# Performance work log

Hardware: AMD Instinct MI355X
Metric: run time of the kernel (lower is better)

Reference implementation:

```python
import jax, jax.numpy as jnp
import numpy as np

B, T, D, H = 2, 2048, 1024, 16
HD = D // H


def setup_inputs() -> dict:
    key = jax.random.key(0)
    ks = jax.random.split(key, 9)
    s = 1.0 / np.sqrt(D)
    return {
        "x": jax.random.normal(ks[0], (B, T, D), dtype=jnp.float32),
        "Wq": jax.random.normal(ks[1], (D, D), dtype=jnp.float32) * s,
        "bq": jnp.zeros((D,), dtype=jnp.float32),
        "Wk": jax.random.normal(ks[2], (D, D), dtype=jnp.float32) * s,
        "bk": jnp.zeros((D,), dtype=jnp.float32),
        "Wv": jax.random.normal(ks[3], (D, D), dtype=jnp.float32) * s,
        "bv": jnp.zeros((D,), dtype=jnp.float32),
        "Wo": jax.random.normal(ks[4], (D, D), dtype=jnp.float32) * s,
        "bo": jnp.zeros((D,), dtype=jnp.float32),
    }


def reference(x, Wq, bq, Wk, bk, Wv, bv, Wo, bo):
    b, t, d = x.shape
    # projections, split heads: (b, h, t, hd)
    def heads(y):
        return y.reshape(b, t, H, HD).transpose(0, 2, 1, 3)
    Q = heads(x @ Wq + bq)
    K = heads(x @ Wk + bk)
    V = heads(x @ Wv + bv)
    # scores scaled by sqrt(d) (full embed dim, faithful to source)
    score = jnp.einsum("bhid,bhjd->bhij", Q, K) / jnp.sqrt(jnp.float32(d))
    causal = jnp.triu(jnp.ones((t, t), dtype=bool), k=1)  # (t, t)
    score = jnp.where(causal, jnp.float32(-1e10), score)
    # FAITHFUL quirk: softmax over the HEAD axis (torch dim=1 of [b,h,t,t])
    weight = jax.nn.softmax(score, axis=1)
    out = jnp.einsum("bhij,bhjd->bhid", weight, V)
    out = out.transpose(0, 2, 1, 3).reshape(b, t, d)
    return out @ Wo + bo
```

## Files before the change

### kernel.cpp

```cpp
#include <hip/hip_runtime.h>
#include <hip/hip_bf16.h>

#define B_ 2
#define T_ 2048
#define D_ 1024
#define H_ 16

typedef __attribute__((ext_vector_type(8))) short bf16x8;
typedef __attribute__((ext_vector_type(4))) short bf16x4;
typedef __attribute__((ext_vector_type(4))) float f32x4;

__device__ __forceinline__ unsigned pack_bf16(float x, float y) {
  unsigned xb = __float_as_uint(x), yb = __float_as_uint(y);
  xb += 0x7fffu + ((xb >> 16) & 1u);
  yb += 0x7fffu + ((yb >> 16) & 1u);
  return (xb >> 16) | (yb & 0xffff0000u);
}
__device__ __forceinline__ unsigned short f2b(float x) {
  unsigned u = __float_as_uint(x);
  u += 0x7fffu + ((u >> 16) & 1u);
  return (unsigned short)(u >> 16);
}
__device__ __forceinline__ float blo(unsigned u) { return __uint_as_float(u << 16); }
__device__ __forceinline__ float bhi(unsigned u) { return __uint_as_float(u & 0xffff0000u); }

__device__ __forceinline__ void gld_lds16(const unsigned short* g, unsigned short* l) {
  __builtin_amdgcn_global_load_lds(
      (const __attribute__((address_space(1))) unsigned int*)g,
      (__attribute__((address_space(3))) unsigned int*)l, 16, 0, 0);
}

__global__ __launch_bounds__(256) void wtrans(const float* __restrict__ W0, const float* __restrict__ W1,
                                              const float* __restrict__ W2, const float* __restrict__ W3,
                                              unsigned short* __restrict__ T0, unsigned short* __restrict__ T1,
                                              unsigned short* __restrict__ T2, unsigned short* __restrict__ T3) {
  const int z = blockIdx.z;
  const float* W = z == 0 ? W0 : z == 1 ? W1 : z == 2 ? W2 : W3;
  unsigned short* T = z == 0 ? T0 : z == 1 ? T1 : z == 2 ? T2 : T3;
  __shared__ unsigned short t[64][72];
  const int k0 = blockIdx.x << 6, n0 = blockIdx.y << 6;
  const int r = threadIdx.x >> 2, c16 = (threadIdx.x & 3) << 4;
#pragma unroll
  for (int e = 0; e < 4; ++e) {
    const float4 v = *(const float4*)&W[(size_t)(k0 + r) * 1024 + n0 + c16 + e * 4];
    t[r][c16 + e * 4 + 0] = f2b(v.x);
    t[r][c16 + e * 4 + 1] = f2b(v.y);
    t[r][c16 + e * 4 + 2] = f2b(v.z);
    t[r][c16 + e * 4 + 3] = f2b(v.w);
  }
  __syncthreads();
  unsigned short o[16];
#pragma unroll
  for (int e = 0; e < 16; ++e) o[e] = t[c16 + e][r];
  unsigned short* dst = &T[(size_t)(n0 + r) * 1024 + k0 + c16];
  *(uint4*)&dst[0] = *(uint4*)&o[0];
  *(uint4*)&dst[8] = *(uint4*)&o[8];
}

__global__ __launch_bounds__(256) void xconv(const float* __restrict__ x, unsigned short* __restrict__ xb) {
  const int i = (blockIdx.x * 256 + threadIdx.x) * 8;
  const float4 a = *(const float4*)&x[i];
  const float4 b = *(const float4*)&x[i + 4];
  uint4 o;
  o.x = pack_bf16(a.x, a.y);
  o.y = pack_bf16(a.z, a.w);
  o.z = pack_bf16(b.x, b.y);
  o.w = pack_bf16(b.z, b.w);
  *(uint4*)&xb[i] = o;
}

template <bool BF16OUT>
__global__ __launch_bounds__(256) void gemm_mfma(const unsigned short* __restrict__ A,
                                                 const unsigned short* __restrict__ B0,
                                                 const unsigned short* __restrict__ B1,
                                                 const unsigned short* __restrict__ B2,
                                                 const float* __restrict__ bi0, const float* __restrict__ bi1,
                                                 const float* __restrict__ bi2,
                                                 void* __restrict__ Y0, void* __restrict__ Y1,
                                                 void* __restrict__ Y2) {
  const int z = blockIdx.z;
  const unsigned short* Bt = z == 0 ? B0 : z == 1 ? B1 : B2;
  const float* bias = z == 0 ? bi0 : z == 1 ? bi1 : bi2;
  void* Y = z == 0 ? Y0 : z == 1 ? Y1 : Y2;
  __shared__ unsigned short As[8192];
  __shared__ unsigned short Bs[8192];
  const int tid = threadIdx.x;
  const int m0 = blockIdx.y << 7, n0 = blockIdx.x << 7;
  const int w = tid >> 6, l = tid & 63, g = l >> 4, c = l & 15;
  const int wm = (w >> 1) << 6, wn = (w & 1) << 6;
  const int srow = tid >> 3;
  const int skel = ((tid & 7) ^ (srow & 7)) << 3;
  const unsigned short* ga = &A[(size_t)(m0 + srow) * 1024 + skel];
  const unsigned short* gb = &Bt[(size_t)(n0 + srow) * 1024 + skel];
  unsigned short* la = &As[tid << 3];
  unsigned short* lb = &Bs[tid << 3];
  f32x4 acc[4][4];
#pragma unroll
  for (int i = 0; i < 4; ++i)
#pragma unroll
    for (int j = 0; j < 4; ++j) acc[i][j] = {0.f, 0.f, 0.f, 0.f};
  for (int k0 = 0; k0 < 1024; k0 += 64) {
    __syncthreads();
#pragma unroll
    for (int a = 0; a < 4; ++a) {
      gld_lds16(ga + (size_t)(a << 5) * 1024 + k0, la + (a << 11));
      gld_lds16(gb + (size_t)(a << 5) * 1024 + k0, lb + (a << 11));
    }
    __syncthreads();
#pragma unroll
    for (int kc = 0; kc < 2; ++kc) {
      bf16x8 af[4], bfr[4];
#pragma unroll
      for (int mf = 0; mf < 4; ++mf) {
        const int m = wm + (mf << 4) + c;
        af[mf] = *(const bf16x8*)&As[((m << 6) + (kc << 5) + (g << 3)) ^ ((m & 7) << 3)];
      }
#pragma unroll
      for (int nf = 0; nf < 4; ++nf) {
        const int n = wn + (nf << 4) + c;
        bfr[nf] = *(const bf16x8*)&Bs[((n << 6) + (kc << 5) + (g << 3)) ^ ((n & 7) << 3)];
      }
#pragma unroll
      for (int mf = 0; mf < 4; ++mf)
#pragma unroll
        for (int nf = 0; nf < 4; ++nf)
          acc[mf][nf] = __builtin_amdgcn_mfma_f32_16x16x32_bf16(af[mf], bfr[nf], acc[mf][nf], 0, 0, 0);
    }
  }
#pragma unroll
  for (int nf = 0; nf < 4; ++nf) {
    const int n = n0 + wn + (nf << 4) + c;
    const float bb = bias[n];
#pragma unroll
    for (int mf = 0; mf < 4; ++mf) {
      const int mrow = m0 + wm + (mf << 4) + (g << 2);
#pragma unroll
      for (int r = 0; r < 4; ++r) {
        const float val = acc[mf][nf][r] + bb;
        if (BF16OUT)
          ((unsigned short*)Y)[((size_t)(mrow + r) << 10) + n] = f2b(val);
        else
          ((float*)Y)[((size_t)(mrow + r) << 10) + n] = val;
      }
    }
  }
}

__global__ __launch_bounds__(256) void gemm_vt(const unsigned short* __restrict__ A,
                                               const unsigned short* __restrict__ Bt,
                                               const float* __restrict__ bias,
                                               unsigned short* __restrict__ Vt) {
  __shared__ unsigned short As[8192];
  __shared__ unsigned short Bs[8192];
  __shared__ unsigned short sm[128][136];
  const int tid = threadIdx.x;
  const int m0 = blockIdx.y << 7, n0 = blockIdx.x << 7;
  const int w = tid >> 6, l = tid & 63, g = l >> 4, c = l & 15;
  const int wm = (w >> 1) << 6, wn = (w & 1) << 6;
  const int srow = tid >> 3;
  const int skel = ((tid & 7) ^ (srow & 7)) << 3;
  const unsigned short* ga = &A[(size_t)(m0 + srow) * 1024 + skel];
  const unsigned short* gb = &Bt[(size_t)(n0 + srow) * 1024 + skel];
  unsigned short* la = &As[tid << 3];
  unsigned short* lb = &Bs[tid << 3];
  f32x4 acc[4][4];
#pragma unroll
  for (int i = 0; i < 4; ++i)
#pragma unroll
    for (int j = 0; j < 4; ++j) acc[i][j] = {0.f, 0.f, 0.f, 0.f};
  for (int k0 = 0; k0 < 1024; k0 += 64) {
    __syncthreads();
#pragma unroll
    for (int a = 0; a < 4; ++a) {
      gld_lds16(ga + (size_t)(a << 5) * 1024 + k0, la + (a << 11));
      gld_lds16(gb + (size_t)(a << 5) * 1024 + k0, lb + (a << 11));
    }
    __syncthreads();
#pragma unroll
    for (int kc = 0; kc < 2; ++kc) {
      bf16x8 af[4], bfr[4];
#pragma unroll
      for (int mf = 0; mf < 4; ++mf) {
        const int m = wm + (mf << 4) + c;
        af[mf] = *(const bf16x8*)&As[((m << 6) + (kc << 5) + (g << 3)) ^ ((m & 7) << 3)];
      }
#pragma unroll
      for (int nf = 0; nf < 4; ++nf) {
        const int n = wn + (nf << 4) + c;
        bfr[nf] = *(const bf16x8*)&Bs[((n << 6) + (kc << 5) + (g << 3)) ^ ((n & 7) << 3)];
      }
#pragma unroll
      for (int mf = 0; mf < 4; ++mf)
#pragma unroll
        for (int nf = 0; nf < 4; ++nf)
          acc[mf][nf] = __builtin_amdgcn_mfma_f32_16x16x32_bf16(af[mf], bfr[nf], acc[mf][nf], 0, 0, 0);
    }
  }
  __syncthreads();
#pragma unroll
  for (int nf = 0; nf < 4; ++nf) {
    const int nl = wn + (nf << 4) + c;
    const float bb = bias[n0 + nl];
#pragma unroll
    for (int mf = 0; mf < 4; ++mf) {
      const int ml = wm + (mf << 4) + (g << 2);
      uint2 o;
      o.x = pack_bf16(acc[mf][nf][0] + bb, acc[mf][nf][1] + bb);
      o.y = pack_bf16(acc[mf][nf][2] + bb, acc[mf][nf][3] + bb);
      *(uint2*)&sm[nl][ml] = o;
    }
  }
  __syncthreads();
  const int bb2 = m0 >> 11, mr0 = m0 & 2047;
#pragma unroll
  for (int it = 0; it < 8; ++it) {
    const int u = tid + (it << 8);
    const int ns = u >> 4, mc = (u & 15) << 3;
    *(uint4*)&Vt[(((size_t)((bb2 << 10) + n0 + ns)) << 11) + mr0 + mc] = *(const uint4*)&sm[ns][mc];
  }
}

__global__ __launch_bounds__(256) void vblk32t(const unsigned short* __restrict__ Vt,
                                               float* __restrict__ Blk) {
  const int b = blockIdx.x >> 6, t = blockIdx.x & 63;
#pragma unroll
  for (int dd = 0; dd < 4; ++dd) {
    const int d = threadIdx.x + (dd << 8);
    const unsigned short* vr = &Vt[(((size_t)((b << 10) + d)) << 11) + (t << 5)];
    float s = 0.f;
#pragma unroll
    for (int qq = 0; qq < 4; ++qq) {
      const uint2 v0 = *(const uint2*)&vr[qq << 3];
      const uint2 v1 = *(const uint2*)&vr[(qq << 3) + 4];
      s += blo(v0.x) + bhi(v0.x) + blo(v0.y) + bhi(v0.y);
      s += blo(v1.x) + bhi(v1.x) + blo(v1.y) + bhi(v1.y);
    }
    Blk[(((size_t)((b << 6) + t)) << 10) + d] = s;
  }
}

__global__ __launch_bounds__(256) void vsuffix32(const float* __restrict__ Blk, float* __restrict__ Suf) {
  const int idx = blockIdx.x * 256 + threadIdx.x;
  const int b = idx >> 10, d = idx & 1023;
  float s = 0.f;
  Suf[((size_t)(b * 65 + 64) << 10) + d] = 0.f;
  for (int t = 63; t >= 0; --t) {
    s += Blk[((size_t)((b << 6) + t) << 10) + d];
    Suf[((size_t)(b * 65 + t) << 10) + d] = s;
  }
}

__global__ __launch_bounds__(1024, 4) void attn_v17(const unsigned short* __restrict__ Qb,
                                                    const unsigned short* __restrict__ Kb,
                                                    const unsigned short* __restrict__ Vt,
                                                    unsigned short* __restrict__ P0,
                                                    unsigned short* __restrict__ P1,
                                                    unsigned short* __restrict__ P2,
                                                    unsigned short* __restrict__ P3) {
  __shared__ unsigned short Ks[2][16 * 1024];
  __shared__ unsigned short Vs[2][1024 * 16];
  __shared__ uint2 Sx[2][8][64];

  const int combo = blockIdx.x;
  const int b = combo & 1, s = combo >> 1;
  const int qy = 63 - blockIdx.y;
  const int tid = threadIdx.x;
  const int w = tid >> 6, l = tid & 63, g = l >> 4, c = l & 15;
  const int isub = w >> 3, hp = w & 7;
  const float SC = 0.04508422f;
  unsigned short* AOp = s == 0 ? P0 : s == 1 ? P1 : s == 2 ? P2 : P3;

  const int krow0 = tid >> 7, kc8 = tid & 127;
  const int kscc0 = kc8 ^ (krow0 & 7);
  const int krow1 = krow0 + 8;
  const int kscc1 = kc8 ^ (krow1 & 7);
  const unsigned short* kp0 = &Kb[(((size_t)((b << 11) + krow0)) << 10) + (kscc0 << 3)];
  const unsigned short* kp1 = &Kb[(((size_t)((b << 11) + krow1)) << 10) + (kscc1 << 3)];
  const int vd0 = tid >> 1, vjc = tid & 1;
  const int vjo0 = ((vjc << 1) ^ (((vd0 >> 2) & 1) << 1)) << 2;
  const int vd1 = vd0 + 512;
  const int vjo1 = ((vjc << 1) ^ (((vd1 >> 2) & 1) << 1)) << 2;
  const unsigned short* vp0 = &Vt[(((size_t)((b << 10) + vd0)) << 11) + vjo0];
  const unsigned short* vp1 = &Vt[(((size_t)((b << 10) + vd1)) << 11) + vjo1];

#pragma unroll
  for (int ph = 0; ph < 2; ++ph) {
    const int q = ph ? (63 - qy) : qy;
    const int nt16 = (q + 1) << 1;
    const int i0w = (q << 5) + (isub << 4);
    const int ib = i0w + c;

    const unsigned short* qbase =
        &Qb[((size_t)((b << 11) + i0w + c) << 10) + (hp << 7) + (g << 3)];
    bf16x8 qf[4];
    qf[0] = *(const bf16x8*)&qbase[0];
    qf[1] = *(const bf16x8*)&qbase[32];
    qf[2] = *(const bf16x8*)&qbase[64];
    qf[3] = *(const bf16x8*)&qbase[96];

    f32x4 acc[2][4];
#pragma unroll
    for (int hh = 0; hh < 2; ++hh)
#pragma unroll
      for (int cc = 0; cc < 4; ++cc) acc[hh][cc] = {0.f, 0.f, 0.f, 0.f};

#pragma unroll
    for (int e = 0; e < 2; ++e) {
      const int eh = e ? (7 - s) : s;
      const int lo = eh << 4;
      const int hi = (lo + 16) < nt16 ? (lo + 16) : nt16;
      if (lo >= hi) continue;

      {
        const size_t ko = ((size_t)lo << 14);
        gld_lds16(kp0 + ko, &Ks[0][tid << 3]);
        gld_lds16(kp1 + ko, &Ks[0][(tid + 1024) << 3]);
        const int jo = lo << 4;
        gld_lds16(vp0 + jo, &Vs[0][tid << 3]);
        gld_lds16(vp1 + jo, &Vs[0][(tid + 1024) << 3]);
      }
      __syncthreads();

      for (int ts = lo; ts < hi; ++ts) {
        const int cur = (ts - lo) & 1;
        if (ts + 1 < hi) {
          const size_t ko = ((size_t)(ts + 1) << 14);
          gld_lds16(kp0 + ko, &Ks[cur ^ 1][tid << 3]);
          gld_lds16(kp1 + ko, &Ks[cur ^ 1][(tid + 1024) << 3]);
          const int jo = (ts + 1) << 4;
          gld_lds16(vp0 + jo, &Vs[cur ^ 1][tid << 3]);
          gld_lds16(vp1 + jo, &Vs[cur ^ 1][(tid + 1024) << 3]);
        }
        const int j0 = ts << 4;
        const int kx = c & 7;
        f32x4 ex[2];
        f32x4 ps = {0.f, 0.f, 0.f, 0.f};
#pragma unroll
        for (int hh = 0; hh < 2; ++hh) {
          const int hc = ((hp << 1) + hh) << 3;
          const bf16x8 k0 = *(const bf16x8*)&Ks[cur][((c << 7) + ((hc + g) ^ kx)) << 3];
          const bf16x8 k1 = *(const bf16x8*)&Ks[cur][((c << 7) + ((hc + 4 + g) ^ kx)) << 3];
          f32x4 a = {0.f, 0.f, 0.f, 0.f};
          a = __builtin_amdgcn_mfma_f32_16x16x32_bf16(k0, qf[2 * hh], a, 0, 0, 0);
          a = __builtin_amdgcn_mfma_f32_16x16x32_bf16(k1, qf[2 * hh + 1], a, 0, 0, 0);
#pragma unroll
          for (int r = 0; r < 4; ++r) ex[hh][r] = exp2f(a[r] * SC);
          ps += ex[hh];
        }
        uint2 pp;
        pp.x = pack_bf16(ps[0], ps[1]);
        pp.y = pack_bf16(ps[2], ps[3]);
        Sx[isub][hp][l] = pp;
        __syncthreads();
        f32x4 sum = {0.f, 0.f, 0.f, 0.f};
#pragma unroll
        for (int d8 = 0; d8 < 8; ++d8) {
          const uint2 u = Sx[isub][d8][l];
          sum[0] += blo(u.x);
          sum[1] += bhi(u.x);
          sum[2] += blo(u.y);
          sum[3] += bhi(u.y);
        }
        f32x4 inv;
#pragma unroll
        for (int r = 0; r < 4; ++r) inv[r] = __builtin_amdgcn_rcpf(sum[r]);
        float wv[2][4];
        if (j0 + 15 <= i0w) {
#pragma unroll
          for (int hh = 0; hh < 2; ++hh)
#pragma unroll
            for (int r = 0; r < 4; ++r) wv[hh][r] = ex[hh][r] * inv[r];
        } else {
          const int jb = j0 + (g << 2);
#pragma unroll
          for (int hh = 0; hh < 2; ++hh)
#pragma unroll
            for (int r = 0; r < 4; ++r)
              wv[hh][r] = (jb + r > ib) ? 0.0625f : ex[hh][r] * inv[r];
        }
#pragma unroll
        for (int hh = 0; hh < 2; ++hh) {
          union { bf16x4 v; unsigned u[2]; } pa;
          pa.u[0] = pack_bf16(wv[hh][0], wv[hh][1]);
          pa.u[1] = pack_bf16(wv[hh][2], wv[hh][3]);
#pragma unroll
          for (int cc = 0; cc < 4; ++cc) {
            const int d = (((hp << 1) + hh) << 6) + (cc << 4) + c;
            const int up = g ^ (((d >> 2) & 1) << 1);
            union { bf16x4 v; unsigned u[2]; } vf;
            *(uint2*)&vf = *(const uint2*)&Vs[cur][(d << 4) + (up << 2)];
            acc[hh][cc] =
                __builtin_amdgcn_mfma_f32_16x16x16bf16_1k(pa.v, vf.v, acc[hh][cc], 0, 0, 0);
          }
        }
        __syncthreads();
      }
    }
#pragma unroll
    for (int hh = 0; hh < 2; ++hh)
#pragma unroll
      for (int cc = 0; cc < 4; ++cc) {
        const int d = (((hp << 1) + hh) << 6) + (cc << 4) + c;
#pragma unroll
        for (int r = 0; r < 4; ++r)
          AOp[((size_t)((b << 11) + i0w + (g << 2) + r) << 10) + d] = f2b(acc[hh][cc][r]);
      }
  }
}

__global__ __launch_bounds__(256) void aocvt(const unsigned short* __restrict__ P0,
                                             const unsigned short* __restrict__ P1,
                                             const unsigned short* __restrict__ P2,
                                             const unsigned short* __restrict__ P3,
                                             const float* __restrict__ Suf,
                                             unsigned short* __restrict__ AOb) {
  const int i = (blockIdx.x * 256 + threadIdx.x) << 3;
  const int m = i >> 10;
  const int b = m >> 11;
  const int sufidx = ((m & 2047) >> 5) + 1;
  const int d0 = i & 1023;
  const float* sp = &Suf[((size_t)(b * 65 + sufidx) << 10) + d0];
  const uint4 v0 = *(const uint4*)&P0[i];
  const uint4 v1 = *(const uint4*)&P1[i];
  const uint4 v2 = *(const uint4*)&P2[i];
  const uint4 v3 = *(const uint4*)&P3[i];
  const float4 s0 = *(const float4*)&sp[0];
  const float4 s1 = *(const float4*)&sp[4];
  uint4 o;
  o.x = pack_bf16(blo(v0.x) + blo(v1.x) + blo(v2.x) + blo(v3.x) + 0.0625f * s0.x,
                  bhi(v0.x) + bhi(v1.x) + bhi(v2.x) + bhi(v3.x) + 0.0625f * s0.y);
  o.y = pack_bf16(blo(v0.y) + blo(v1.y) + blo(v2.y) + blo(v3.y) + 0.0625f * s0.z,
                  bhi(v0.y) + bhi(v1.y) + bhi(v2.y) + bhi(v3.y) + 0.0625f * s0.w);
  o.z = pack_bf16(blo(v0.z) + blo(v1.z) + blo(v2.z) + blo(v3.z) + 0.0625f * s1.x,
                  bhi(v0.z) + bhi(v1.z) + bhi(v2.z) + bhi(v3.z) + 0.0625f * s1.y);
  o.w = pack_bf16(blo(v0.w) + blo(v1.w) + blo(v2.w) + blo(v3.w) + 0.0625f * s1.z,
                  bhi(v0.w) + bhi(v1.w) + bhi(v2.w) + bhi(v3.w) + 0.0625f * s1.w);
  *(uint4*)&AOb[i] = o;
}

extern "C" void kernel_launch(void* const* d_in, const int* in_sizes, int n_in,
                              void* d_out, int out_size, void* d_ws, size_t ws_size,
                              hipStream_t stream) {
  (void)in_sizes; (void)n_in; (void)out_size; (void)ws_size;
  const float* x = (const float*)d_in[0];
  const float* Wq = (const float*)d_in[1];
  const float* bq = (const float*)d_in[2];
  const float* Wk = (const float*)d_in[3];
  const float* bk = (const float*)d_in[4];
  const float* Wv = (const float*)d_in[5];
  const float* bv = (const float*)d_in[6];
  const float* Wo = (const float*)d_in[7];
  const float* bo = (const float*)d_in[8];
  float* out = (float*)d_out;
  char* ws = (char*)d_ws;

  const size_t MB = 1024 * 1024;
  unsigned short* xb  = (unsigned short*)(ws);
  unsigned short* Qb  = (unsigned short*)(ws + 8 * MB);
  unsigned short* Kb  = (unsigned short*)(ws + 16 * MB);
  unsigned short* AOP1 = (unsigned short*)(ws + 24 * MB);
  unsigned short* Vt  = (unsigned short*)(ws + 32 * MB);
  unsigned short* Wqt = (unsigned short*)(ws + 40 * MB);
  unsigned short* Wkt = (unsigned short*)(ws + 42 * MB);
  unsigned short* Wvt = (unsigned short*)(ws + 44 * MB);
  unsigned short* Wot = (unsigned short*)(ws + 46 * MB);
  unsigned short* AOP2 = (unsigned short*)(ws + 48 * MB);
  unsigned short* AOP3 = (unsigned short*)(ws + 56 * MB);
  float* Blk = (float*)(ws + 40 * MB);
  float* Suf = (float*)(ws + 40 * MB + 512 * 1024);
  unsigned short* AOP0 = xb;
  unsigned short* AOb = Qb;

  hipLaunchKernelGGL(wtrans, dim3(16, 16, 4), dim3(256), 0, stream,
                     Wq, Wk, Wv, Wo, Wqt, Wkt, Wvt, Wot);
  hipLaunchKernelGGL(xconv, dim3(2048), dim3(256), 0, stream, x, xb);
  hipLaunchKernelGGL((gemm_mfma<true>), dim3(8, 32, 2), dim3(256), 0, stream,
                     xb, Wqt, Wkt, Wkt, bq, bk, bk, (void*)Qb, (void*)Kb, (void*)Kb);
  hipLaunchKernelGGL(gemm_vt, dim3(8, 32), dim3(256), 0, stream, xb, Wvt, bv, Vt);
  hipLaunchKernelGGL(vblk32t, dim3(128), dim3(256), 0, stream, Vt, Blk);
  hipLaunchKernelGGL(vsuffix32, dim3(8), dim3(256), 0, stream, Blk, Suf);
  hipLaunchKernelGGL(attn_v17, dim3(8, 32), dim3(1024), 0, stream,
                     Qb, Kb, Vt, AOP0, AOP1, AOP2, AOP3);
  hipLaunchKernelGGL(aocvt, dim3(2048), dim3(256), 0, stream,
                     AOP0, AOP1, AOP2, AOP3, Suf, AOb);
  hipLaunchKernelGGL((gemm_mfma<false>), dim3(8, 32, 1), dim3(256), 0, stream,
                     AOb, Wot, Wot, Wot, bo, bo, bo, (void*)out, (void*)out, (void*)out);
}
```

Measured before the change: 196.0 us.

## Fuse partial-sum reduction into output GEMM and use fp32 head-sum exchange

Removes the separate aocvt pass by folding the reduction of the four attention partial outputs plus the suffix term into the A-tile load of a new output-projection GEMM. This drops one kernel launch and one write and read of the combined activation buffer. Each A tile is now rebuilt from four partial buffers in every N-block, so those reads are repeated eight times. The attention kernel also exchanges per-head exp sums in fp32 instead of packed bf16, using a raw barrier with an explicit waitcnt. This costs twice the shared memory for that buffer but skips the pack and unpack work.

```diff
diff --git a/kernel.cpp b/kernel.cpp
--- a/kernel.cpp
+++ b/kernel.cpp
@@ -250,7 +250,7 @@
   }
 }
 
-__global__ __launch_bounds__(1024, 4) void attn_v17(const unsigned short* __restrict__ Qb,
+__global__ __launch_bounds__(1024, 4) void attn_v18(const unsigned short* __restrict__ Qb,
                                                     const unsigned short* __restrict__ Kb,
                                                     const unsigned short* __restrict__ Vt,
                                                     unsigned short* __restrict__ P0,
@@ -259,7 +259,7 @@
                                                     unsigned short* __restrict__ P3) {
   __shared__ unsigned short Ks[2][16 * 1024];
   __shared__ unsigned short Vs[2][1024 * 16];
-  __shared__ uint2 Sx[2][8][64];
+  __shared__ f32x4 Sx[2][8][64];
 
   const int combo = blockIdx.x;
   const int b = combo & 1, s = combo >> 1;
@@ -347,20 +347,13 @@
           for (int r = 0; r < 4; ++r) ex[hh][r] = exp2f(a[r] * SC);
           ps += ex[hh];
         }
-        uint2 pp;
-        pp.x = pack_bf16(ps[0], ps[1]);
-        pp.y = pack_bf16(ps[2], ps[3]);
-        Sx[isub][hp][l] = pp;
-        __syncthreads();
-        f32x4 sum = {0.f, 0.f, 0.f, 0.f};
-#pragma unroll
-        for (int d8 = 0; d8 < 8; ++d8) {
-          const uint2 u = Sx[isub][d8][l];
-          sum[0] += blo(u.x);
-          sum[1] += bhi(u.x);
-          sum[2] += blo(u.y);
-          sum[3] += bhi(u.y);
-        }
+        Sx[isub][hp][l] = ps;
+        asm volatile("s_waitcnt lgkmcnt(0)" ::: "memory");
+        __builtin_amdgcn_s_barrier();
+        __builtin_amdgcn_sched_barrier(0);
+        f32x4 sum = Sx[isub][0][l];
+#pragma unroll
+        for (int d8 = 1; d8 < 8; ++d8) sum += Sx[isub][d8][l];
         f32x4 inv;
 #pragma unroll
         for (int r = 0; r < 4; ++r) inv[r] = __builtin_amdgcn_rcpf(sum[r]);
@@ -408,34 +401,96 @@
   }
 }
 
-__global__ __launch_bounds__(256) void aocvt(const unsigned short* __restrict__ P0,
-                                             const unsigned short* __restrict__ P1,
-                                             const unsigned short* __restrict__ P2,
-                                             const unsigned short* __restrict__ P3,
-                                             const float* __restrict__ Suf,
-                                             unsigned short* __restrict__ AOb) {
-  const int i = (blockIdx.x * 256 + threadIdx.x) << 3;
-  const int m = i >> 10;
-  const int b = m >> 11;
-  const int sufidx = ((m & 2047) >> 5) + 1;
-  const int d0 = i & 1023;
-  const float* sp = &Suf[((size_t)(b * 65 + sufidx) << 10) + d0];
-  const uint4 v0 = *(const uint4*)&P0[i];
-  const uint4 v1 = *(const uint4*)&P1[i];
-  const uint4 v2 = *(const uint4*)&P2[i];
-  const uint4 v3 = *(const uint4*)&P3[i];
-  const float4 s0 = *(const float4*)&sp[0];
-  const float4 s1 = *(const float4*)&sp[4];
-  uint4 o;
-  o.x = pack_bf16(blo(v0.x) + blo(v1.x) + blo(v2.x) + blo(v3.x) + 0.0625f * s0.x,
-                  bhi(v0.x) + bhi(v1.x) + bhi(v2.x) + bhi(v3.x) + 0.0625f * s0.y);
-  o.y = pack_bf16(blo(v0.y) + blo(v1.y) + blo(v2.y) + blo(v3.y) + 0.0625f * s0.z,
-                  bhi(v0.y) + bhi(v1.y) + bhi(v2.y) + bhi(v3.y) + 0.0625f * s0.w);
-  o.z = pack_bf16(blo(v0.z) + blo(v1.z) + blo(v2.z) + blo(v3.z) + 0.0625f * s1.x,
-                  bhi(v0.z) + bhi(v1.z) + bhi(v2.z) + bhi(v3.z) + 0.0625f * s1.y);
-  o.w = pack_bf16(blo(v0.w) + blo(v1.w) + blo(v2.w) + blo(v3.w) + 0.0625f * s1.z,
-                  bhi(v0.w) + bhi(v1.w) + bhi(v2.w) + bhi(v3.w) + 0.0625f * s1.w);
-  *(uint4*)&AOb[i] = o;
+__global__ __launch_bounds__(256) void gemm_out(const unsigned short* __restrict__ P0,
+                                                const unsigned short* __restrict__ P1,
+                                                const unsigned short* __restrict__ P2,
+                                                const unsigned short* __restrict__ P3,
+                                                const float* __restrict__ Suf,
+                                                const unsigned short* __restrict__ Bt,
+                                                const float* __restrict__ bias,
+                                                float* __restrict__ Y) {
+  __shared__ unsigned short As[8192];
+  __shared__ unsigned short Bs[8192];
+  const int tid = threadIdx.x;
+  const int m0 = blockIdx.y << 7, n0 = blockIdx.x << 7;
+  const int w = tid >> 6, l = tid & 63, g = l >> 4, c = l & 15;
+  const int wm = (w >> 1) << 6, wn = (w & 1) << 6;
+  const int srow = tid >> 3;
+  const int skel = ((tid & 7) ^ (srow & 7)) << 3;
+  const unsigned short* gb = &Bt[(size_t)(n0 + srow) * 1024 + skel];
+  unsigned short* lb = &Bs[tid << 3];
+  size_t abase[4];
+  const float* sufp[4];
+#pragma unroll
+  for (int a = 0; a < 4; ++a) {
+    const int m = m0 + srow + (a << 5);
+    abase[a] = ((size_t)m << 10) + skel;
+    const int b2 = m >> 11;
+    const int sufidx = ((m & 2047) >> 5) + 1;
+    sufp[a] = &Suf[((size_t)(b2 * 65 + sufidx) << 10) + skel];
+  }
+  f32x4 acc[4][4];
+#pragma unroll
+  for (int i = 0; i < 4; ++i)
+#pragma unroll
+    for (int j = 0; j < 4; ++j) acc[i][j] = {0.f, 0.f, 0.f, 0.f};
+  for (int k0 = 0; k0 < 1024; k0 += 64) {
+    __syncthreads();
+#pragma unroll
+    for (int a = 0; a < 4; ++a) {
+      const size_t base = abase[a] + k0;
+      const uint4 v0 = *(const uint4*)&P0[base];
+      const uint4 v1 = *(const uint4*)&P1[base];
+      const uint4 v2 = *(const uint4*)&P2[base];
+      const uint4 v3 = *(const uint4*)&P3[base];
+      const float* sp = sufp[a] + k0;
+      const float4 sA = *(const float4*)&sp[0];
+      const float4 sB = *(const float4*)&sp[4];
+      uint4 o;
+      o.x = pack_bf16(blo(v0.x) + blo(v1.x) + blo(v2.x) + blo(v3.x) + 0.0625f * sA.x,
+                      bhi(v0.x) + bhi(v1.x) + bhi(v2.x) + bhi(v3.x) + 0.0625f * sA.y);
+      o.y = pack_bf16(blo(v0.y) + blo(v1.y) + blo(v2.y) + blo(v3.y) + 0.0625f * sA.z,
+                      bhi(v0.y) + bhi(v1.y) + bhi(v2.y) + bhi(v3.y) + 0.0625f * sA.w);
+      o.z = pack_bf16(blo(v0.z) + blo(v1.z) + blo(v2.z) + blo(v3.z) + 0.0625f * sB.x,
+                      bhi(v0.z) + bhi(v1.z) + bhi(v2.z) + bhi(v3.z) + 0.0625f * sB.y);
+      o.w = pack_bf16(blo(v0.w) + blo(v1.w) + blo(v2.w) + blo(v3.w) + 0.0625f * sB.z,
+                      bhi(v0.w) + bhi(v1.w) + bhi(v2.w) + bhi(v3.w) + 0.0625f * sB.w);
+      *(uint4*)&As[(tid << 3) + (a << 11)] = o;
+      gld_lds16(gb + (size_t)(a << 5) * 1024 + k0, lb + (a << 11));
+    }
+    __syncthreads();
+#pragma unroll
+    for (int kc = 0; kc < 2; ++kc) {
+      bf16x8 af[4], bfr[4];
+#pragma unroll
+      for (int mf = 0; mf < 4; ++mf) {
+        const int m = wm + (mf << 4) + c;
+        af[mf] = *(const bf16x8*)&As[((m << 6) + (kc << 5) + (g << 3)) ^ ((m & 7) << 3)];
+      }
+#pragma unroll
+      for (int nf = 0; nf < 4; ++nf) {
+        const int n = wn + (nf << 4) + c;
+        bfr[nf] = *(const bf16x8*)&Bs[((n << 6) + (kc << 5) + (g << 3)) ^ ((n & 7) << 3)];
+      }
+#pragma unroll
+      for (int mf = 0; mf < 4; ++mf)
+#pragma unroll
+        for (int nf = 0; nf < 4; ++nf)
+          acc[mf][nf] = __builtin_amdgcn_mfma_f32_16x16x32_bf16(af[mf], bfr[nf], acc[mf][nf], 0, 0, 0);
+    }
+  }
+#pragma unroll
+  for (int nf = 0; nf < 4; ++nf) {
+    const int n = n0 + wn + (nf << 4) + c;
+    const float bb = bias[n];
+#pragma unroll
+    for (int mf = 0; mf < 4; ++mf) {
+      const int mrow = m0 + wm + (mf << 4) + (g << 2);
+#pragma unroll
+      for (int r = 0; r < 4; ++r)
+        Y[((size_t)(mrow + r) << 10) + n] = acc[mf][nf][r] + bb;
+    }
+  }
 }
 
 extern "C" void kernel_launch(void* const* d_in, const int* in_sizes, int n_in,
@@ -469,7 +524,6 @@
   float* Blk = (float*)(ws + 40 * MB);
   float* Suf = (float*)(ws + 40 * MB + 512 * 1024);
   unsigned short* AOP0 = xb;
-  unsigned short* AOb = Qb;
 
   hipLaunchKernelGGL(wtrans, dim3(16, 16, 4), dim3(256), 0, stream,
                      Wq, Wk, Wv, Wo, Wqt, Wkt, Wvt, Wot);
@@ -479,10 +533,8 @@
   hipLaunchKernelGGL(gemm_vt, dim3(8, 32), dim3(256), 0, stream, xb, Wvt, bv, Vt);
   hipLaunchKernelGGL(vblk32t, dim3(128), dim3(256), 0, stream, Vt, Blk);
   hipLaunchKernelGGL(vsuffix32, dim3(8), dim3(256), 0, stream, Blk, Suf);
-  hipLaunchKernelGGL(attn_v17, dim3(8, 32), dim3(1024), 0, stream,
+  hipLaunchKernelGGL(attn_v18, dim3(8, 32), dim3(1024), 0, stream,
                      Qb, Kb, Vt, AOP0, AOP1, AOP2, AOP3);
-  hipLaunchKernelGGL(aocvt, dim3(2048), dim3(256), 0, stream,
-                     AOP0, AOP1, AOP2, AOP3, Suf, AOb);
-  hipLaunchKernelGGL((gemm_mfma<false>), dim3(8, 32, 1), dim3(256), 0, stream,
-                     AOb, Wot, Wot, Wot, bo, bo, bo, (void*)out, (void*)out, (void*)out);
-}
+  hipLaunchKernelGGL(gemm_out, dim3(8, 32), dim3(256), 0, stream,
+                     AOP0, AOP1, AOP2, AOP3, Suf, Wot, bo, out);
+}
```

New measurement: 226.3 us. +15.5%, slower.
